# Optimization experiments

Measured on AMD Instinct MI355X. Metric: run time of the kernel, lower is better.

The kernel has to match this reference:

```python
import jax, jax.numpy as jnp
import numpy as np

S = 41          # seq_len
D_IN = 1280
D_OUT = 1024
HEADS = 4
HC = D_OUT // HEADS
EPS = 1e-5

# ---- static edge construction (faithful to the torch code, incl. duplicate edges) ----

def _local_edges(s, window=1):
    e = []
    for i in range(s):
        for j in range(max(0, i - window), min(s, i + window + 1)):
            if i != j:
                e += [(i, j), (j, i)]
    return np.array(e, dtype=np.int32).T

def _region_edges(s):
    e = []
    step = s // 3
    for st in range(0, s, step):
        blk = range(st, min(st + step, s))
        for i in blk:
            for j in blk:
                if i != j:
                    e += [(i, j), (j, i)]
    return np.array(e, dtype=np.int32).T

def _global_edges(s):
    r, c = np.triu_indices(s, 1)  # torch.combinations: (i, j) with i < j
    return np.stack([r, c]).astype(np.int32)

def _batch_edges(e, b, s):
    off = np.arange(b, dtype=np.int32) * s
    return (e[:, None, :] + off[None, :, None]).reshape(2, -1)

_LOCAL = _local_edges(S)
_REGION = _region_edges(S)
_GLOBAL = _global_edges(S)

# ---- layer primitives ----

def _layernorm(x, g, b):
    mu = x.mean(-1, keepdims=True)
    v = ((x - mu) ** 2).mean(-1, keepdims=True)
    return (x - mu) / jnp.sqrt(v + EPS) * g + b

def _gcn(x, w, b, src, tgt, n):
    # PyG GCNConv: x' = D^-1/2 (A + I) D^-1/2 (x W) + b
    h = x @ w
    sl = jnp.arange(n, dtype=src.dtype)
    s = jnp.concatenate([src, sl]); t = jnp.concatenate([tgt, sl])
    deg = jax.ops.segment_sum(jnp.ones(t.shape, h.dtype), t, n)
    dinv = jnp.where(deg > 0, jax.lax.rsqrt(jnp.maximum(deg, 1.0)), 0.0)
    norm = dinv[s] * dinv[t]
    return jax.ops.segment_sum(h[s] * norm[:, None], t, n) + b

def _gat(x, w, a_src, a_dst, b, src, tgt, n):
    # PyG GATConv (shared lin, self loops, leaky_relu 0.2, softmax over incoming edges)
    h = (x @ w).reshape(n, HEADS, HC)
    sl = jnp.arange(n, dtype=src.dtype)
    s = jnp.concatenate([src, sl]); t = jnp.concatenate([tgt, sl])
    al_s = (h * a_src).sum(-1)  # [n, H]
    al_d = (h * a_dst).sum(-1)
    e = jax.nn.leaky_relu(al_s[s] + al_d[t], 0.2)  # [E, H]
    m = jax.ops.segment_max(e, t, n)
    ex = jnp.exp(e - m[t])
    den = jax.ops.segment_sum(ex, t, n)
    alpha = ex / den[t]
    out = jax.ops.segment_sum(h[s] * alpha[:, :, None], t, n)
    return out.reshape(n, HEADS * HC) + b

def _sage(x, wl, bl, wr, src, tgt, n):
    # PyG SAGEConv: mean-aggregate neighbors, plus root transform
    cnt = jax.ops.segment_sum(jnp.ones(src.shape, x.dtype), tgt, n)
    agg = jax.ops.segment_sum(x[src], tgt, n) / jnp.maximum(cnt, 1.0)[:, None]
    return agg @ wl + bl + x @ wr


def setup_inputs() -> dict:
    key = jax.random.key(0)
    ks = jax.random.split(key, 16)
    sc = 0.02
    f32 = jnp.float32
    inp = {
        'x': jax.random.normal(ks[0], (512, S, D_IN), f32),
        'att_w': jax.random.normal(ks[1], (D_IN, 1), f32) * sc,
        'att_b': jnp.zeros((1,), f32),
        'gcn_w': jax.random.normal(ks[2], (D_IN, D_OUT), f32) * sc,
        'gcn_b': jnp.zeros((D_OUT,), f32),
        'sn_g': jnp.ones((D_OUT,), f32), 'sn_b': jnp.zeros((D_OUT,), f32),
        'gat_w': jax.random.normal(ks[3], (D_IN, D_OUT), f32) * sc,
        'gat_as': jax.random.normal(ks[4], (HEADS, HC), f32) * sc,
        'gat_ad': jax.random.normal(ks[5], (HEADS, HC), f32) * sc,
        'gat_b': jnp.zeros((D_OUT,), f32),
        'mn_g': jnp.ones((D_OUT,), f32), 'mn_b': jnp.zeros((D_OUT,), f32),
        'sage_wl': jax.random.normal(ks[6], (D_IN, D_OUT), f32) * sc,
        'sage_bl': jnp.zeros((D_OUT,), f32),
        'sage_wr': jax.random.normal(ks[7], (D_IN, D_OUT), f32) * sc,
        'fp_w1': jax.random.normal(ks[8], (D_IN, 512), f32) * sc,
        'fp_b1': jnp.zeros((512,), f32),
        'fp_w2': jax.random.normal(ks[9], (512, S), f32) * sc,
        'fp_b2': jnp.zeros((S,), f32),
        'dn_g': jnp.ones((D_OUT,), f32), 'dn_b': jnp.zeros((D_OUT,), f32),
        'gate_w': jax.random.normal(ks[10], (3 * D_OUT, 3), f32) * sc,
        'gate_b': jnp.zeros((3,), f32),
    }
    return inp


def reference(x, att_w, att_b, gcn_w, gcn_b, sn_g, sn_b, gat_w, gat_as, gat_ad, gat_b,
              mn_g, mn_b, sage_wl, sage_bl, sage_wr, fp_w1, fp_b1, fp_w2, fp_b2,
              dn_g, dn_b, gate_w, gate_b):
    B = x.shape[0]
    N = B * S
    le = jnp.asarray(_batch_edges(_LOCAL, B, S))
    re = jnp.asarray(_batch_edges(_REGION, B, S))
    ge = jnp.asarray(_batch_edges(_GLOBAL, B, S))

    xf = x.reshape(N, D_IN)
    # shallow: local gating -> GCN -> LN
    enhanced = xf * jax.nn.sigmoid(xf @ att_w + att_b)
    shallow = _gcn(enhanced, gcn_w, gcn_b, le[0], le[1], N)
    shallow = _layernorm(shallow.reshape(B, S, D_OUT), sn_g, sn_b)
    # medium: GAT over region blocks -> LN
    gat = _gat(xf, gat_w, gat_as[None], gat_ad[None], gat_b, re[0], re[1], N)
    gat = _layernorm(gat.reshape(B, S, D_OUT), mn_g, mn_b)
    # deep: learned propagation mixing, SAGE over global edges -> LN
    pw = jax.nn.softmax(jax.nn.relu(x @ fp_w1 + fp_b1) @ fp_w2 + fp_b2, axis=-1)  # [B,S,S]
    sage_in = jnp.einsum('bij,bjd->bid', pw, x).reshape(N, D_IN)
    sage = _sage(sage_in, sage_wl, sage_bl, sage_wr, ge[0], ge[1], N)
    sage = _layernorm(sage.reshape(B, S, D_OUT), dn_g, dn_b)
    # gated branch mixing
    combined = jnp.concatenate([shallow, gat, sage], axis=-1)
    gates = jax.nn.softmax(combined @ gate_w + gate_b, axis=-1)
    total = gates[..., 0:1] * shallow + gates[..., 1:2] * gat + gates[..., 2:3] * sage
    return (shallow, gat, total)
```

## Files before the change

kernel.cpp:

```cpp
#include <hip/hip_runtime.h>
#include <math.h>

static constexpr int S    = 41;
static constexpr int DIN  = 1280;
static constexpr int DOUT = 1024;
static constexpr int HEADS = 4;
static constexpr int HC   = 256;

typedef __attribute__((ext_vector_type(4))) float f32x4;
typedef __attribute__((ext_vector_type(8))) short short8;

__device__ __forceinline__ ushort f2bf(float f) {
  uint u = __float_as_uint(f);
  uint r = u + 0x7fffu + ((u >> 16) & 1u);
  return (ushort)(r >> 16);
}
__device__ __forceinline__ float bf2f(ushort u) {
  return __uint_as_float(((uint)u) << 16);
}

__device__ __forceinline__ void gload16(const ushort* g, ushort* l) {
  __builtin_amdgcn_global_load_lds((const __attribute__((address_space(1))) void*)g,
                                   (__attribute__((address_space(3))) void*)l, 16, 0, 0);
}

#define FENCE() asm volatile("" ::: "memory")


__device__ __forceinline__ float warpReduceSum(float v) {
#pragma unroll
  for (int off = 32; off; off >>= 1) v += __shfl_down(v, off);
  return v;
}

__device__ __forceinline__ void blockReduce6(float* v) {
  __shared__ float red6[6][4];
  int w = threadIdx.x >> 6, lane = threadIdx.x & 63;
#pragma unroll
  for (int r = 0; r < 6; ++r) v[r] = warpReduceSum(v[r]);
  __syncthreads();
  if (lane == 0) {
#pragma unroll
    for (int r = 0; r < 6; ++r) red6[r][w] = v[r];
  }
  __syncthreads();
#pragma unroll
  for (int r = 0; r < 6; ++r)
    v[r] = red6[r][0] + red6[r][1] + red6[r][2] + red6[r][3];
}

__device__ __forceinline__ void blockReduce3v(float* v) {
  __shared__ float red3[3][4];
  int w = threadIdx.x >> 6, lane = threadIdx.x & 63;
#pragma unroll
  for (int r = 0; r < 3; ++r) v[r] = warpReduceSum(v[r]);
  __syncthreads();
  if (lane == 0) {
#pragma unroll
    for (int r = 0; r < 3; ++r) red3[r][w] = v[r];
  }
  __syncthreads();
#pragma unroll
  for (int r = 0; r < 3; ++r)
    v[r] = red3[r][0] + red3[r][1] + red3[r][2] + red3[r][3];
}


__global__ __launch_bounds__(256) void cvtsig_kernel(
    const float4* __restrict__ x, const float* __restrict__ att_w,
    const float* __restrict__ att_b, ushort4* __restrict__ xb, float* __restrict__ sig)
{
  int row  = blockIdx.x * 4 + (threadIdx.x >> 6);
  int lane = threadIdx.x & 63;
  const float4* xr = x + (size_t)row * (DIN / 4);
  const float4* wr = (const float4*)att_w;
  ushort4* xo = xb + (size_t)row * (DIN / 4);
  float acc = 0.f;
#pragma unroll
  for (int k = 0; k < DIN / 4 / 64; ++k) {
    float4 a = xr[lane + k * 64];
    float4 w = wr[lane + k * 64];
    acc += a.x * w.x + a.y * w.y + a.z * w.z + a.w * w.w;
    ushort4 o;
    o.x = f2bf(a.x); o.y = f2bf(a.y); o.z = f2bf(a.z); o.w = f2bf(a.w);
    xo[lane + k * 64] = o;
  }
  acc = warpReduceSum(acc);
  if (lane == 0) sig[row] = 1.f / (1.f + expf(-(acc + att_b[0])));
}


__global__ __launch_bounds__(256) void wcvt_kernel(const float* __restrict__ W,
                                                   ushort* __restrict__ out,
                                                   int K, int N, int ostride, int koff) {
  __shared__ float t[32][33];
  int n0 = blockIdx.x * 32, k0 = blockIdx.y * 32;
  int tx = threadIdx.x & 31, ty = threadIdx.x >> 5;
#pragma unroll
  for (int r = 0; r < 4; ++r) {
    int k = ty + r * 8;
    t[k][tx] = W[(size_t)(k0 + k) * N + n0 + tx];
  }
  __syncthreads();
#pragma unroll
  for (int r = 0; r < 4; ++r) {
    int nn = ty + r * 8;
    out[(size_t)(n0 + nn) * ostride + koff + k0 + tx] = f2bf(t[tx][nn]);
  }
}

__global__ __launch_bounds__(256) void w2cvt_kernel(const float* __restrict__ w2,
                                                    ushort* __restrict__ wpw) {
  int idx = blockIdx.x * 256 + threadIdx.x;
  int n = idx >> 9, k = idx & 511;
  wpw[idx] = (n < S) ? f2bf(w2[(size_t)k * S + n]) : (ushort)0;
}


struct Epi {
  void* dst[5];
  const float* bias[5];
  int nend[5];
  int ld[5];
  int relu[5];
  const float* rs;
};


__global__ __launch_bounds__(512, 1) void gemm8p(
    const ushort* __restrict__ A, const ushort* __restrict__ Bt, int K, int nb, Epi e)
{
  __shared__ __align__(16) ushort As[4 * 8192];
  __shared__ __align__(16) ushort Bs[4 * 8192];

  int wg;
  {
    const int nwg = gridDim.x;
    const int bid = blockIdx.x;
    const int xcd = bid & 7, lin = bid >> 3;
    const int q = nwg >> 3, r = nwg & 7;
    wg = (xcd < r) ? (xcd * (q + 1) + lin) : (r * (q + 1) + (xcd - r) * q + lin);
  }
  const int bm = (wg / nb) * 256;
  const int bn = (wg % nb) * 256;

  const int tid  = threadIdx.x;
  const int wv   = tid >> 6;
  const int lane = tid & 63;
  const int l16  = lane & 15;
  const int l4   = lane >> 4;
  const int m0   = (wv >> 2) * 128;
  const int n0   = (wv & 3) * 64;

  const int rd0 = wv * 16 + (lane >> 2);
  const int rd1 = 128 + wv * 16 + (lane >> 2);
  const int cs0 = ((lane & 3) - ((rd0 >> 1) & 3)) & 3;
  const int cs1 = ((lane & 3) - ((rd1 >> 1) & 3)) & 3;

  auto stageA = [&](int h, int Tt) {
    int kof = Tt * 64 + (h & 1) * 32;
    gload16(A + (size_t)(bm + rd0) * K + kof + cs0 * 8, &As[h * 8192 + wv * 512]);
    gload16(A + (size_t)(bm + rd1) * K + kof + cs1 * 8, &As[h * 8192 + (8 + wv) * 512]);
  };
  auto stageB = [&](int h, int Tt) {
    int kof = Tt * 64 + (h & 1) * 32;
    gload16(Bt + (size_t)(bn + rd0) * K + kof + cs0 * 8, &Bs[h * 8192 + wv * 512]);
    gload16(Bt + (size_t)(bn + rd1) * K + kof + cs1 * 8, &Bs[h * 8192 + (8 + wv) * 512]);
  };

  const int rchunk = ((l4 + ((l16 >> 1) & 3)) & 3) * 8;

  f32x4 acc[8][4];
#pragma unroll
  for (int i = 0; i < 8; ++i)
#pragma unroll
    for (int j = 0; j < 4; ++j) acc[i][j] = (f32x4)0.f;

  const int NT = K >> 6;

  stageA(0, 0); stageB(0, 0);
  stageA(1, 0); stageB(1, 0);
  stageA(2, 1); stageB(2, 1);
  asm volatile("s_waitcnt vmcnt(8)" ::: "memory");
  __builtin_amdgcn_s_barrier();
  FENCE();

  for (int T = 0; T < NT; ++T) {
    const int db = T & 1;
    const int hA = db * 2;
    const int hB = db * 2 + 1;
    short8 a[4], b[4];

#pragma unroll
    for (int i = 0; i < 4; ++i)
      a[i] = *reinterpret_cast<const short8*>(&As[hA * 8192 + (m0 + i * 16 + l16) * 32 + rchunk]);
#pragma unroll
    for (int j = 0; j < 4; ++j)
      b[j] = *reinterpret_cast<const short8*>(&Bs[hA * 8192 + (n0 + j * 16 + l16) * 32 + rchunk]);
    if (T + 1 < NT) stageA((db ^ 1) * 2 + 1, T + 1);
    FENCE(); __builtin_amdgcn_s_barrier(); FENCE();
    __builtin_amdgcn_s_setprio(1);
#pragma unroll
    for (int i = 0; i < 4; ++i)
#pragma unroll
      for (int j = 0; j < 4; ++j)
        acc[i][j] = __builtin_amdgcn_mfma_f32_16x16x32_bf16(a[i], b[j], acc[i][j], 0, 0, 0);
    __builtin_amdgcn_s_setprio(0);
    FENCE(); __builtin_amdgcn_s_barrier(); FENCE();

#pragma unroll
    for (int i = 0; i < 4; ++i)
      a[i] = *reinterpret_cast<const short8*>(&As[hA * 8192 + (m0 + 64 + i * 16 + l16) * 32 + rchunk]);
    if (T + 1 < NT) {
      stageB((db ^ 1) * 2 + 1, T + 1);
      asm volatile("s_waitcnt vmcnt(8)" ::: "memory");
    } else {
      asm volatile("s_waitcnt vmcnt(0)" ::: "memory");
    }
    FENCE(); __builtin_amdgcn_s_barrier(); FENCE();
    __builtin_amdgcn_s_setprio(1);
#pragma unroll
    for (int i = 0; i < 4; ++i)
#pragma unroll
      for (int j = 0; j < 4; ++j)
        acc[4 + i][j] = __builtin_amdgcn_mfma_f32_16x16x32_bf16(a[i], b[j], acc[4 + i][j], 0, 0, 0);
    __builtin_amdgcn_s_setprio(0);
    FENCE(); __builtin_amdgcn_s_barrier(); FENCE();

#pragma unroll
    for (int i = 0; i < 4; ++i)
      a[i] = *reinterpret_cast<const short8*>(&As[hB * 8192 + (m0 + i * 16 + l16) * 32 + rchunk]);
#pragma unroll
    for (int j = 0; j < 4; ++j)
      b[j] = *reinterpret_cast<const short8*>(&Bs[hB * 8192 + (n0 + j * 16 + l16) * 32 + rchunk]);
    if (T + 2 < NT) stageA(hA, T + 2);
    FENCE(); __builtin_amdgcn_s_barrier(); FENCE();
    __builtin_amdgcn_s_setprio(1);
#pragma unroll
    for (int i = 0; i < 4; ++i)
#pragma unroll
      for (int j = 0; j < 4; ++j)
        acc[i][j] = __builtin_amdgcn_mfma_f32_16x16x32_bf16(a[i], b[j], acc[i][j], 0, 0, 0);
    __builtin_amdgcn_s_setprio(0);
    FENCE(); __builtin_amdgcn_s_barrier(); FENCE();

#pragma unroll
    for (int i = 0; i < 4; ++i)
      a[i] = *reinterpret_cast<const short8*>(&As[hB * 8192 + (m0 + 64 + i * 16 + l16) * 32 + rchunk]);
    if (T + 2 < NT) {
      stageB(hA, T + 2);
      asm volatile("s_waitcnt vmcnt(8)" ::: "memory");
    } else if (T + 1 < NT) {
      asm volatile("s_waitcnt vmcnt(4)" ::: "memory");
    }
    FENCE(); __builtin_amdgcn_s_barrier(); FENCE();
    __builtin_amdgcn_s_setprio(1);
#pragma unroll
    for (int i = 0; i < 4; ++i)
#pragma unroll
      for (int j = 0; j < 4; ++j)
        acc[4 + i][j] = __builtin_amdgcn_mfma_f32_16x16x32_bf16(a[i], b[j], acc[4 + i][j], 0, 0, 0);
    __builtin_amdgcn_s_setprio(0);
    FENCE(); __builtin_amdgcn_s_barrier(); FENCE();
  }

  void* dstv; const float* bias; const float* rs = nullptr; int ldc, cb, relu;
  if (bn < e.nend[0])      { dstv = e.dst[0]; ldc = e.ld[0]; cb = bn;             bias = e.bias[0]; relu = e.relu[0]; rs = e.rs; }
  else if (bn < e.nend[1]) { dstv = e.dst[1]; ldc = e.ld[1]; cb = bn - e.nend[0]; bias = e.bias[1]; relu = e.relu[1]; }
  else if (bn < e.nend[2]) { dstv = e.dst[2]; ldc = e.ld[2]; cb = bn - e.nend[1]; bias = e.bias[2]; relu = e.relu[2]; }
  else if (bn < e.nend[3]) { dstv = e.dst[3]; ldc = e.ld[3]; cb = bn - e.nend[2]; bias = e.bias[3]; relu = e.relu[3]; }
  else                     { dstv = e.dst[4]; ldc = e.ld[4]; cb = bn - e.nend[3]; bias = e.bias[4]; relu = e.relu[4]; }

#pragma unroll
  for (int i = 0; i < 8; ++i) {
    int mbase = bm + m0 + i * 16 + l4 * 4;
    float rsv[4];
#pragma unroll
    for (int r = 0; r < 4; ++r) rsv[r] = rs ? rs[mbase + r] : 1.f;
#pragma unroll
    for (int j = 0; j < 4; ++j) {
      int col = cb + n0 + j * 16 + l16;
      float bv = bias ? bias[col] : 0.f;
#pragma unroll
      for (int r = 0; r < 4; ++r) {
        float t = acc[i][j][r] * rsv[r] + bv;
        if (relu) t = fmaxf(t, 0.f);
        ((ushort*)dstv)[(size_t)(mbase + r) * ldc + col] = f2bf(t);
      }
    }
  }
}


template<bool F32OUT>
__global__ __launch_bounds__(256) void gemm_bf16(
    const ushort* __restrict__ A, const ushort* __restrict__ Bt, int K, int nb, Epi e)
{
  __shared__ __align__(16) ushort As[3][128 * 32];
  __shared__ __align__(16) ushort Bs[3][128 * 32];

  const int bid = blockIdx.x;
  const int bm  = (bid / nb) * 128;
  const int bn  = (bid % nb) * 128;

  const int tid  = threadIdx.x;
  const int w    = tid >> 6;
  const int lane = tid & 63;
  const int l16  = lane & 15;
  const int l4   = lane >> 4;
  const int m0   = (w >> 1) * 64;
  const int n0   = (w & 1) * 64;

  const int rloc = lane >> 2;
  const int cpos = lane & 3;
  const int cdat = (cpos - (rloc >> 1)) & 3;
  const int srow = w * 32 + rloc;
  const int scol = cdat * 8;

  f32x4 acc[4][4];
#pragma unroll
  for (int i = 0; i < 4; ++i)
#pragma unroll
    for (int j = 0; j < 4; ++j) acc[i][j] = (f32x4)0.f;

  const ushort* pA0 = A  + (size_t)(bm + srow) * K + scol;
  const ushort* pA1 = A  + (size_t)(bm + srow + 16) * K + scol;
  const ushort* pB0 = Bt + (size_t)(bn + srow) * K + scol;
  const ushort* pB1 = Bt + (size_t)(bn + srow + 16) * K + scol;

  auto stage = [&](int buf, int kt) {
    gload16(pA0 + kt, &As[buf][w * 1024]);
    gload16(pA1 + kt, &As[buf][w * 1024 + 512]);
    gload16(pB0 + kt, &Bs[buf][w * 1024]);
    gload16(pB1 + kt, &Bs[buf][w * 1024 + 512]);
  };

  const int rchunk = ((l4 + (l16 >> 1)) & 3) * 8;

  const int nsteps = K >> 5;
  stage(0, 0); stage(1, 32); stage(2, 64);

  for (int t = 0; t < nsteps; ++t) {
    if (t == 0)                asm volatile("s_waitcnt vmcnt(8)" ::: "memory");
    else if (t == nsteps - 1)  asm volatile("s_waitcnt vmcnt(0)" ::: "memory");
    else                       asm volatile("s_waitcnt vmcnt(4)" ::: "memory");
    __builtin_amdgcn_s_barrier();
    FENCE();

    if (t >= 1 && t + 2 < nsteps) stage((t + 2) % 3, (t + 2) * 32);

    const int cur = t % 3;
    short8 a[4], b[4];
#pragma unroll
    for (int i = 0; i < 4; ++i)
      a[i] = *reinterpret_cast<const short8*>(&As[cur][(m0 + i * 16 + l16) * 32 + rchunk]);
#pragma unroll
    for (int j = 0; j < 4; ++j)
      b[j] = *reinterpret_cast<const short8*>(&Bs[cur][(n0 + j * 16 + l16) * 32 + rchunk]);
    __builtin_amdgcn_s_setprio(1);
#pragma unroll
    for (int i = 0; i < 4; ++i)
#pragma unroll
      for (int j = 0; j < 4; ++j)
        acc[i][j] = __builtin_amdgcn_mfma_f32_16x16x32_bf16(a[i], b[j], acc[i][j], 0, 0, 0);
    __builtin_amdgcn_s_setprio(0);
  }

  void* dstv; const float* bias; const float* rs = nullptr; int ldc, cb, relu;
  if (bn < e.nend[0])      { dstv = e.dst[0]; ldc = e.ld[0]; cb = bn;             bias = e.bias[0]; relu = e.relu[0]; rs = e.rs; }
  else if (bn < e.nend[1]) { dstv = e.dst[1]; ldc = e.ld[1]; cb = bn - e.nend[0]; bias = e.bias[1]; relu = e.relu[1]; }
  else if (bn < e.nend[2]) { dstv = e.dst[2]; ldc = e.ld[2]; cb = bn - e.nend[1]; bias = e.bias[2]; relu = e.relu[2]; }
  else if (bn < e.nend[3]) { dstv = e.dst[3]; ldc = e.ld[3]; cb = bn - e.nend[2]; bias = e.bias[3]; relu = e.relu[3]; }
  else                     { dstv = e.dst[4]; ldc = e.ld[4]; cb = bn - e.nend[3]; bias = e.bias[4]; relu = e.relu[4]; }

#pragma unroll
  for (int i = 0; i < 4; ++i) {
    int mbase = bm + m0 + i * 16 + l4 * 4;
    float rsv[4];
#pragma unroll
    for (int r = 0; r < 4; ++r) rsv[r] = rs ? rs[mbase + r] : 1.f;
#pragma unroll
    for (int j = 0; j < 4; ++j) {
      int col = cb + n0 + j * 16 + l16;
      float bv = bias ? bias[col] : 0.f;
#pragma unroll
      for (int r = 0; r < 4; ++r) {
        float t = acc[i][j][r] * rsv[r] + bv;
        if (relu) t = fmaxf(t, 0.f);
        if (F32OUT) ((float*)dstv)[(size_t)(mbase + r) * ldc + col] = t;
        else        ((ushort*)dstv)[(size_t)(mbase + r) * ldc + col] = f2bf(t);
      }
    }
  }
}


__global__ __launch_bounds__(256) void pwprep_kernel(
    const float* __restrict__ fp2, const float* __restrict__ fp_b2,
    float* __restrict__ pc)
{
  int b = blockIdx.x;
  int tid = threadIdx.x, wv = tid >> 6, lane = tid & 63;
  __shared__ float pws[S][S];
  for (int i = wv; i < S; i += 4) {
    float v = (lane < S) ? (fp2[(size_t)(b * S + i) * 128 + lane] + fp_b2[lane]) : -1e30f;
    float m = v;
#pragma unroll
    for (int off = 32; off; off >>= 1) m = fmaxf(m, __shfl_xor(m, off));
    float e = (lane < S) ? expf(v - m) : 0.f;
    float sum = e;
#pragma unroll
    for (int off = 32; off; off >>= 1) sum += __shfl_xor(sum, off);
    if (lane < S) {
      float p = e / sum;
      pws[i][lane] = p;
      pc[((size_t)b * S + i) * 128 + lane] = p;
    }
  }
  __syncthreads();
  if (tid < S) {
    float run = 0.f;
    for (int i = 0; i < S; ++i) {
      pc[((size_t)b * S + i) * 128 + 64 + tid] = (i > 0) ? run / (float)i : 0.f;
      run += pws[i][tid];
    }
  }
}


__global__ __launch_bounds__(256) void mixc_kernel(
    const float* __restrict__ pc, const ushort* __restrict__ xr,
    const ushort* __restrict__ xl, const float* __restrict__ sage_bl,
    ushort* __restrict__ hbuf)
{
  int b  = blockIdx.y;
  int d0 = blockIdx.x * 256;
  int tid = threadIdx.x;

  float xrv[S], xlv[S];
  const ushort* xrp = xr + (size_t)(b * S) * DOUT + d0 + tid;
  const ushort* xlp = xl + (size_t)(b * S) * DOUT + d0 + tid;
#pragma unroll
  for (int j = 0; j < S; ++j) {
    xrv[j] = bf2f(xrp[(size_t)j * DOUT]);
    xlv[j] = bf2f(xlp[(size_t)j * DOUT]);
  }
  float bl = sage_bl[d0 + tid];
  ushort* op = hbuf + (size_t)(b * S) * DOUT + d0 + tid;
  const float* pcb = pc + (size_t)(b * S) * 128;
  for (int i = 0; i < S; ++i) {
    const float* row = pcb + (size_t)i * 128;
    float acc = bl;
#pragma unroll
    for (int j = 0; j < S; ++j)
      acc += row[j] * xrv[j] + row[64 + j] * xlv[j];
    op[(size_t)i * DOUT] = f2bf(acc);
  }
}


__device__ __forceinline__ float dinv_local(int j) {
  return rsqrtf((j == 0 || j == S - 1) ? 3.f : 5.f);
}

__global__ __launch_bounds__(256) void tail_fused(
    const ushort* __restrict__ gcnh, const ushort* __restrict__ Cgat,
    const ushort* __restrict__ hbuf,
    const float* __restrict__ gcn_b, const float* __restrict__ sn_g, const float* __restrict__ sn_b,
    const float* __restrict__ gat_as, const float* __restrict__ gat_ad, const float* __restrict__ gat_b,
    const float* __restrict__ mn_g, const float* __restrict__ mn_b,
    const float* __restrict__ dn_g, const float* __restrict__ dn_b,
    const float* __restrict__ gw, const float* __restrict__ gb,
    float* __restrict__ out, int N)
{
  int b  = blockIdx.x >> 2;
  int rb = blockIdx.x & 3;
  int lo = rb * 13;
  int cnt = (rb < 3) ? 13 : 2;
  size_t OUT = (size_t)N * DOUT;
  int tid = threadIdx.x;
  int wv = tid >> 6, lane = tid & 63;
  int d0 = tid * 4;
  int head = tid >> 6;

  __shared__ __align__(16) ushort hs[13][DOUT];
  __shared__ float alpha[13][13][HEADS];
  __shared__ float als_l[13][HEADS], ald_l[13][HEADS];

  for (int r = 0; r < cnt; ++r) {
    const ushort4* src = (const ushort4*)(Cgat + (size_t)(b * S + lo + r) * DOUT);
    ((ushort4*)hs[r])[tid] = src[tid];
  }
  __syncthreads();

  {
    const float4* a4 = (const float4*)(gat_as + wv * HC);
    const float4* d4 = (const float4*)(gat_ad + wv * HC);
    float4 av = a4[lane], dv = d4[lane];
    for (int s = 0; s < cnt; ++s) {
      ushort4 hv4 = ((const ushort4*)&hs[s][wv * HC])[lane];
      float h0 = bf2f(hv4.x), h1 = bf2f(hv4.y), h2 = bf2f(hv4.z), h3 = bf2f(hv4.w);
      float a = h0 * av.x + h1 * av.y + h2 * av.z + h3 * av.w;
      float d = h0 * dv.x + h1 * dv.y + h2 * dv.z + h3 * dv.w;
      a = warpReduceSum(a);
      d = warpReduceSum(d);
      if (lane == 0) { als_l[s][wv] = a; ald_l[s][wv] = d; }
    }
  }
  __syncthreads();

  if (tid < cnt * HEADS) {
    int t = tid >> 2, hd = tid & 3;
    float myald = ald_l[t][hd];
    float m = -1e30f;
    for (int s = 0; s < cnt; ++s) {
      float v = als_l[s][hd] + myald;
      v = (v > 0.f) ? v : 0.2f * v;
      m = fmaxf(m, v);
    }
    float den = 0.f;
    for (int s = 0; s < cnt; ++s) {
      float v = als_l[s][hd] + myald;
      v = (v > 0.f) ? v : 0.2f * v;
      float ev = expf(v - m) * ((s == t) ? 1.f : 2.f);
      alpha[t][s][hd] = ev;
      den += ev;
    }
    float inv = 1.f / den;
    for (int s = 0; s < cnt; ++s) alpha[t][s][hd] *= inv;
  }
  __syncthreads();

  float4 gcnb4 = *(const float4*)(gcn_b + d0);
  float4 sng4  = *(const float4*)(sn_g + d0);
  float4 snb4  = *(const float4*)(sn_b + d0);
  float4 gatb4 = *(const float4*)(gat_b + d0);
  float4 mng4  = *(const float4*)(mn_g + d0);
  float4 mnb4  = *(const float4*)(mn_b + d0);
  float4 dng4  = *(const float4*)(dn_g + d0);
  float4 dnb4  = *(const float4*)(dn_b + d0);
  float gwsh[4][3], gwga[4][3], gwsa[4][3];
#pragma unroll
  for (int q = 0; q < 4; ++q)
#pragma unroll
    for (int c = 0; c < 3; ++c) {
      gwsh[q][c] = gw[(size_t)(d0 + q) * 3 + c];
      gwga[q][c] = gw[(size_t)(DOUT + d0 + q) * 3 + c];
      gwsa[q][c] = gw[(size_t)(2 * DOUT + d0 + q) * 3 + c];
    }

  for (int t = 0; t < cnt; ++t) {
    int i = lo + t;
    size_t n = (size_t)(b * S + i);

    float di = dinv_local(i);
    float wc = di * di;
    float wl = (i > 0)     ? 2.f * di * dinv_local(i - 1) : 0.f;
    float wr = (i < S - 1) ? 2.f * di * dinv_local(i + 1) : 0.f;
    const ushort* hc = gcnh + n * DOUT + d0;
    ushort4 c4  = *(const ushort4*)hc;
    ushort4 lft = (i > 0)     ? *(const ushort4*)(hc - DOUT) : ushort4{0, 0, 0, 0};
    ushort4 rgt = (i < S - 1) ? *(const ushort4*)(hc + DOUT) : ushort4{0, 0, 0, 0};
    const ushort* cp = (const ushort*)&c4;
    const ushort* lp = (const ushort*)&lft;
    const ushort* rp = (const ushort*)&rgt;
    const float* gbp = (const float*)&gcnb4;
    float sh[4];
#pragma unroll
    for (int q = 0; q < 4; ++q)
      sh[q] = wc * bf2f(cp[q]) + wl * bf2f(lp[q]) + wr * bf2f(rp[q]) + gbp[q];

    float ga[4] = {0.f, 0.f, 0.f, 0.f};
    for (int si = 0; si < cnt; ++si) {
      float aj = alpha[t][si][head];
      ushort4 hv = *(const ushort4*)&hs[si][d0];
      ga[0] += aj * bf2f(hv.x);
      ga[1] += aj * bf2f(hv.y);
      ga[2] += aj * bf2f(hv.z);
      ga[3] += aj * bf2f(hv.w);
    }
    const float* gab = (const float*)&gatb4;
#pragma unroll
    for (int q = 0; q < 4; ++q) ga[q] += gab[q];

    ushort4 s4v = *(const ushort4*)(hbuf + n * DOUT + d0);
    const ushort* sp = (const ushort*)&s4v;
    float sa[4];
#pragma unroll
    for (int q = 0; q < 4; ++q) sa[q] = bf2f(sp[q]);

    float red[6] = {0.f, 0.f, 0.f, 0.f, 0.f, 0.f};
#pragma unroll
    for (int q = 0; q < 4; ++q) {
      red[0] += sh[q]; red[1] += sh[q] * sh[q];
      red[2] += ga[q]; red[3] += ga[q] * ga[q];
      red[4] += sa[q]; red[5] += sa[q] * sa[q];
    }
    blockReduce6(red);
    float mu0 = red[0] * (1.f / DOUT), r0 = rsqrtf(red[1] * (1.f / DOUT) - mu0 * mu0 + 1e-5f);
    float mu1 = red[2] * (1.f / DOUT), r1 = rsqrtf(red[3] * (1.f / DOUT) - mu1 * mu1 + 1e-5f);
    float mu2 = red[4] * (1.f / DOUT), r2 = rsqrtf(red[5] * (1.f / DOUT) - mu2 * mu2 + 1e-5f);

    const float* sngp = (const float*)&sng4; const float* snbp = (const float*)&snb4;
    const float* mngp = (const float*)&mng4; const float* mnbp = (const float*)&mnb4;
    const float* dngp = (const float*)&dng4; const float* dnbp = (const float*)&dnb4;
    float shn[4], gan[4], san[4];
#pragma unroll
    for (int q = 0; q < 4; ++q) {
      shn[q] = (sh[q] - mu0) * r0 * sngp[q] + snbp[q];
      gan[q] = (ga[q] - mu1) * r1 * mngp[q] + mnbp[q];
      san[q] = (sa[q] - mu2) * r2 * dngp[q] + dnbp[q];
    }

    float p[3] = {0.f, 0.f, 0.f};
#pragma unroll
    for (int q = 0; q < 4; ++q) {
#pragma unroll
      for (int c = 0; c < 3; ++c)
        p[c] += shn[q] * gwsh[q][c] + gan[q] * gwga[q][c] + san[q] * gwsa[q][c];
    }
    blockReduce3v(p);
    float l0 = p[0] + gb[0], l1 = p[1] + gb[1], l2 = p[2] + gb[2];
    float m = fmaxf(l0, fmaxf(l1, l2));
    float e0 = expf(l0 - m), e1 = expf(l1 - m), e2 = expf(l2 - m);
    float inv = 1.f / (e0 + e1 + e2);
    float g0 = e0 * inv, g1 = e1 * inv, g2 = e2 * inv;

    float4 o0, o1, o2;
    float* o0p = (float*)&o0; float* o1p = (float*)&o1; float* o2p = (float*)&o2;
#pragma unroll
    for (int q = 0; q < 4; ++q) {
      o0p[q] = shn[q];
      o1p[q] = gan[q];
      o2p[q] = g0 * shn[q] + g1 * gan[q] + g2 * san[q];
    }
    *(float4*)(out + n * DOUT + d0)           = o0;
    *(float4*)(out + OUT + n * DOUT + d0)     = o1;
    *(float4*)(out + 2 * OUT + n * DOUT + d0) = o2;
  }
}


extern "C" void kernel_launch(void* const* d_in, const int* in_sizes, int n_in,
                              void* d_out, int out_size, void* d_ws, size_t ws_size,
                              hipStream_t stream) {
  const float* x       = (const float*)d_in[0];
  const float* att_w   = (const float*)d_in[1];
  const float* att_b   = (const float*)d_in[2];
  const float* gcn_w   = (const float*)d_in[3];
  const float* gcn_b   = (const float*)d_in[4];
  const float* sn_g    = (const float*)d_in[5];
  const float* sn_b    = (const float*)d_in[6];
  const float* gat_w   = (const float*)d_in[7];
  const float* gat_as  = (const float*)d_in[8];
  const float* gat_ad  = (const float*)d_in[9];
  const float* gat_b   = (const float*)d_in[10];
  const float* mn_g    = (const float*)d_in[11];
  const float* mn_b    = (const float*)d_in[12];
  const float* sage_wl = (const float*)d_in[13];
  const float* sage_bl = (const float*)d_in[14];
  const float* sage_wr = (const float*)d_in[15];
  const float* fp_w1   = (const float*)d_in[16];
  const float* fp_b1   = (const float*)d_in[17];
  const float* fp_w2   = (const float*)d_in[18];
  const float* fp_b2   = (const float*)d_in[19];
  const float* dn_g    = (const float*)d_in[20];
  const float* dn_b    = (const float*)d_in[21];
  const float* gate_w  = (const float*)d_in[22];
  const float* gate_b  = (const float*)d_in[23];

  const int B = in_sizes[0] / (S * DIN);
  const int N = B * S;
  const int MB  = N / 128;
  const int MB2 = N / 256;
  const int NMEGA = 4608;
  float* out = (float*)d_out;

  char* ws = (char*)d_ws;
  size_t off = 0;
  auto alloc = [&](size_t bytes) { size_t p = off; off += (bytes + 255) & ~(size_t)255; return p; };
  ushort* xb   = (ushort*)(ws + alloc((size_t)N * DIN * 2));
  ushort* Bt   = (ushort*)(ws + alloc((size_t)NMEGA * DIN * 2));
  ushort* wpw  = (ushort*)(ws + alloc((size_t)128 * 512 * 2));
  ushort* gcnh = (ushort*)(ws + alloc((size_t)N * DOUT * 2));
  ushort* Cgat = (ushort*)(ws + alloc((size_t)N * DOUT * 2));
  ushort* xr   = (ushort*)(ws + alloc((size_t)N * DOUT * 2));
  ushort* xl   = (ushort*)(ws + alloc((size_t)N * DOUT * 2));
  ushort* hbuf = (ushort*)(ws + alloc((size_t)N * DOUT * 2));
  float*  fp2  = (float*)(ws + alloc((size_t)N * 128 * 4));
  float*  pc   = (float*)(ws + alloc((size_t)N * 128 * 4));
  float*  sig  = (float*)(ws + alloc((size_t)N * 4));
  ushort* fp1  = hbuf;

  dim3 blk(256);

  cvtsig_kernel<<<N / 4, blk, 0, stream>>>((const float4*)x, att_w, att_b, (ushort4*)xb, sig);
  wcvt_kernel<<<dim3(DOUT / 32, DIN / 32), blk, 0, stream>>>(gcn_w, Bt, DIN, DOUT, DIN, 0);
  wcvt_kernel<<<dim3(DOUT / 32, DIN / 32), blk, 0, stream>>>(gat_w, Bt + (size_t)1024 * DIN, DIN, DOUT, DIN, 0);
  wcvt_kernel<<<dim3(512 / 32, DIN / 32), blk, 0, stream>>>(fp_w1, Bt + (size_t)2048 * DIN, DIN, 512, DIN, 0);
  wcvt_kernel<<<dim3(DOUT / 32, DIN / 32), blk, 0, stream>>>(sage_wr, Bt + (size_t)2560 * DIN, DIN, DOUT, DIN, 0);
  wcvt_kernel<<<dim3(DOUT / 32, DIN / 32), blk, 0, stream>>>(sage_wl, Bt + (size_t)3584 * DIN, DIN, DOUT, DIN, 0);
  w2cvt_kernel<<<dim3(128 * 512 / 256), blk, 0, stream>>>(fp_w2, wpw);

  Epi e1;
  e1.dst[0] = gcnh; e1.dst[1] = Cgat; e1.dst[2] = fp1; e1.dst[3] = xr; e1.dst[4] = xl;
  e1.bias[0] = nullptr; e1.bias[1] = nullptr; e1.bias[2] = fp_b1; e1.bias[3] = nullptr; e1.bias[4] = nullptr;
  e1.nend[0] = 1024; e1.nend[1] = 2048; e1.nend[2] = 2560; e1.nend[3] = 3584; e1.nend[4] = 4608;
  e1.ld[0] = DOUT; e1.ld[1] = DOUT; e1.ld[2] = 512; e1.ld[3] = DOUT; e1.ld[4] = DOUT;
  e1.relu[0] = 0; e1.relu[1] = 0; e1.relu[2] = 1; e1.relu[3] = 0; e1.relu[4] = 0;
  e1.rs = sig;
  gemm8p<<<dim3(MB2 * (NMEGA / 256)), dim3(512), 0, stream>>>(xb, Bt, DIN, NMEGA / 256, e1);

  Epi epw;
  epw.dst[0] = fp2; epw.dst[1] = nullptr; epw.dst[2] = nullptr; epw.dst[3] = nullptr; epw.dst[4] = nullptr;
  epw.bias[0] = nullptr; epw.bias[1] = nullptr; epw.bias[2] = nullptr; epw.bias[3] = nullptr; epw.bias[4] = nullptr;
  epw.nend[0] = 1 << 30; epw.nend[1] = 1 << 30; epw.nend[2] = 1 << 30; epw.nend[3] = 1 << 30; epw.nend[4] = 1 << 30;
  epw.ld[0] = 128; epw.ld[1] = 128; epw.ld[2] = 128; epw.ld[3] = 128; epw.ld[4] = 128;
  epw.relu[0] = 0; epw.relu[1] = 0; epw.relu[2] = 0; epw.relu[3] = 0; epw.relu[4] = 0;
  epw.rs = nullptr;
  gemm_bf16<true><<<dim3(MB), blk, 0, stream>>>(fp1, wpw, 512, 1, epw);

  pwprep_kernel<<<B, blk, 0, stream>>>(fp2, fp_b2, pc);
  mixc_kernel<<<dim3(DOUT / 256, B), blk, 0, stream>>>(pc, xr, xl, sage_bl, hbuf);

  tail_fused<<<B * 4, blk, 0, stream>>>(gcnh, Cgat, hbuf,
                                        gcn_b, sn_g, sn_b,
                                        gat_as, gat_ad, gat_b,
                                        mn_g, mn_b, dn_g, dn_b,
                                        gate_w, gate_b, out, N);
}
```

Baseline: 652.1 us.

## Batch weight conversions, unroll GEMM k-loop by two, and trim reduction barriers

Four weight-transpose launches are merged into one wcvt4 launch that picks its matrix from blockIdx.z. The GEMM main loop is unrolled by two with a constant double-buffer index, and global addresses are precomputed once outside the loop. The final epilogue block reductions use parity-indexed (double-buffered) shared scratch, which drops one __syncthreads per reduction. These target launch overhead, address arithmetic and barrier cost, but the two-way unroll assumes the tile count K/64 is even.

```diff
diff --git a/kernel.cpp b/kernel.cpp
--- a/kernel.cpp
+++ b/kernel.cpp
@@ -31,38 +31,6 @@
 #pragma unroll
   for (int off = 32; off; off >>= 1) v += __shfl_down(v, off);
   return v;
-}
-
-__device__ __forceinline__ void blockReduce6(float* v) {
-  __shared__ float red6[6][4];
-  int w = threadIdx.x >> 6, lane = threadIdx.x & 63;
-#pragma unroll
-  for (int r = 0; r < 6; ++r) v[r] = warpReduceSum(v[r]);
-  __syncthreads();
-  if (lane == 0) {
-#pragma unroll
-    for (int r = 0; r < 6; ++r) red6[r][w] = v[r];
-  }
-  __syncthreads();
-#pragma unroll
-  for (int r = 0; r < 6; ++r)
-    v[r] = red6[r][0] + red6[r][1] + red6[r][2] + red6[r][3];
-}
-
-__device__ __forceinline__ void blockReduce3v(float* v) {
-  __shared__ float red3[3][4];
-  int w = threadIdx.x >> 6, lane = threadIdx.x & 63;
-#pragma unroll
-  for (int r = 0; r < 3; ++r) v[r] = warpReduceSum(v[r]);
-  __syncthreads();
-  if (lane == 0) {
-#pragma unroll
-    for (int r = 0; r < 3; ++r) red3[r][w] = v[r];
-  }
-  __syncthreads();
-#pragma unroll
-  for (int r = 0; r < 3; ++r)
-    v[r] = red3[r][0] + red3[r][1] + red3[r][2] + red3[r][3];
 }
 
 
@@ -90,6 +58,27 @@
 }
 
 
+struct W4 { const float* src[4]; ushort* dst[4]; };
+
+__global__ __launch_bounds__(256) void wcvt4_kernel(W4 w) {
+  __shared__ float t[32][33];
+  const float* W = w.src[blockIdx.z];
+  ushort* out = w.dst[blockIdx.z];
+  int n0 = blockIdx.x * 32, k0 = blockIdx.y * 32;
+  int tx = threadIdx.x & 31, ty = threadIdx.x >> 5;
+#pragma unroll
+  for (int r = 0; r < 4; ++r) {
+    int k = ty + r * 8;
+    t[k][tx] = W[(size_t)(k0 + k) * DOUT + n0 + tx];
+  }
+  __syncthreads();
+#pragma unroll
+  for (int r = 0; r < 4; ++r) {
+    int nn = ty + r * 8;
+    out[(size_t)(n0 + nn) * DIN + k0 + tx] = f2bf(t[tx][nn]);
+  }
+}
+
 __global__ __launch_bounds__(256) void wcvt_kernel(const float* __restrict__ W,
                                                    ushort* __restrict__ out,
                                                    int K, int N, int ostride, int koff) {
@@ -157,15 +146,18 @@
   const int cs0 = ((lane & 3) - ((rd0 >> 1) & 3)) & 3;
   const int cs1 = ((lane & 3) - ((rd1 >> 1) & 3)) & 3;
 
-  auto stageA = [&](int h, int Tt) {
-    int kof = Tt * 64 + (h & 1) * 32;
-    gload16(A + (size_t)(bm + rd0) * K + kof + cs0 * 8, &As[h * 8192 + wv * 512]);
-    gload16(A + (size_t)(bm + rd1) * K + kof + cs1 * 8, &As[h * 8192 + (8 + wv) * 512]);
+  const ushort* gA0 = A  + (size_t)(bm + rd0) * K + cs0 * 8;
+  const ushort* gA1 = A  + (size_t)(bm + rd1) * K + cs1 * 8;
+  const ushort* gB0 = Bt + (size_t)(bn + rd0) * K + cs0 * 8;
+  const ushort* gB1 = Bt + (size_t)(bn + rd1) * K + cs1 * 8;
+
+  auto stageA = [&](int h, int kof) {
+    gload16(gA0 + kof, &As[h * 8192 + wv * 512]);
+    gload16(gA1 + kof, &As[h * 8192 + (8 + wv) * 512]);
   };
-  auto stageB = [&](int h, int Tt) {
-    int kof = Tt * 64 + (h & 1) * 32;
-    gload16(Bt + (size_t)(bn + rd0) * K + kof + cs0 * 8, &Bs[h * 8192 + wv * 512]);
-    gload16(Bt + (size_t)(bn + rd1) * K + kof + cs1 * 8, &Bs[h * 8192 + (8 + wv) * 512]);
+  auto stageB = [&](int h, int kof) {
+    gload16(gB0 + kof, &Bs[h * 8192 + wv * 512]);
+    gload16(gB1 + kof, &Bs[h * 8192 + (8 + wv) * 512]);
   };
 
   const int rchunk = ((l4 + ((l16 >> 1) & 3)) & 3) * 8;
@@ -178,15 +170,14 @@
 
   const int NT = K >> 6;
 
-  stageA(0, 0); stageB(0, 0);
-  stageA(1, 0); stageB(1, 0);
-  stageA(2, 1); stageB(2, 1);
+  stageA(0, 0);  stageB(0, 0);
+  stageA(1, 32); stageB(1, 32);
+  stageA(2, 64); stageB(2, 64);
   asm volatile("s_waitcnt vmcnt(8)" ::: "memory");
   __builtin_amdgcn_s_barrier();
   FENCE();
 
-  for (int T = 0; T < NT; ++T) {
-    const int db = T & 1;
+  auto tileBody = [&](int T, const int db) {
     const int hA = db * 2;
     const int hB = db * 2 + 1;
     short8 a[4], b[4];
@@ -197,7 +188,7 @@
 #pragma unroll
     for (int j = 0; j < 4; ++j)
       b[j] = *reinterpret_cast<const short8*>(&Bs[hA * 8192 + (n0 + j * 16 + l16) * 32 + rchunk]);
-    if (T + 1 < NT) stageA((db ^ 1) * 2 + 1, T + 1);
+    if (T + 1 < NT) stageA((db ^ 1) * 2 + 1, (T + 1) * 64 + 32);
     FENCE(); __builtin_amdgcn_s_barrier(); FENCE();
     __builtin_amdgcn_s_setprio(1);
 #pragma unroll
@@ -212,7 +203,7 @@
     for (int i = 0; i < 4; ++i)
       a[i] = *reinterpret_cast<const short8*>(&As[hA * 8192 + (m0 + 64 + i * 16 + l16) * 32 + rchunk]);
     if (T + 1 < NT) {
-      stageB((db ^ 1) * 2 + 1, T + 1);
+      stageB((db ^ 1) * 2 + 1, (T + 1) * 64 + 32);
       asm volatile("s_waitcnt vmcnt(8)" ::: "memory");
     } else {
       asm volatile("s_waitcnt vmcnt(0)" ::: "memory");
@@ -233,7 +224,7 @@
 #pragma unroll
     for (int j = 0; j < 4; ++j)
       b[j] = *reinterpret_cast<const short8*>(&Bs[hB * 8192 + (n0 + j * 16 + l16) * 32 + rchunk]);
-    if (T + 2 < NT) stageA(hA, T + 2);
+    if (T + 2 < NT) stageA(hA, (T + 2) * 64);
     FENCE(); __builtin_amdgcn_s_barrier(); FENCE();
     __builtin_amdgcn_s_setprio(1);
 #pragma unroll
@@ -248,7 +239,7 @@
     for (int i = 0; i < 4; ++i)
       a[i] = *reinterpret_cast<const short8*>(&As[hB * 8192 + (m0 + 64 + i * 16 + l16) * 32 + rchunk]);
     if (T + 2 < NT) {
-      stageB(hA, T + 2);
+      stageB(hA, (T + 2) * 64);
       asm volatile("s_waitcnt vmcnt(8)" ::: "memory");
     } else if (T + 1 < NT) {
       asm volatile("s_waitcnt vmcnt(4)" ::: "memory");
@@ -262,6 +253,11 @@
         acc[4 + i][j] = __builtin_amdgcn_mfma_f32_16x16x32_bf16(a[i], b[j], acc[4 + i][j], 0, 0, 0);
     __builtin_amdgcn_s_setprio(0);
     FENCE(); __builtin_amdgcn_s_barrier(); FENCE();
+  };
+
+  for (int T = 0; T < NT; T += 2) {
+    tileBody(T, 0);
+    tileBody(T + 1, 1);
   }
 
   void* dstv; const float* bias; const float* rs = nullptr; int ldc, cb, relu;
@@ -486,6 +482,8 @@
   __shared__ __align__(16) ushort hs[13][DOUT];
   __shared__ float alpha[13][13][HEADS];
   __shared__ float als_l[13][HEADS], ald_l[13][HEADS];
+  __shared__ float red6[2][6][4];
+  __shared__ float red3[2][3][4];
 
   for (int r = 0; r < cnt; ++r) {
     const ushort4* src = (const ushort4*)(Cgat + (size_t)(b * S + lo + r) * DOUT);
@@ -552,6 +550,7 @@
   for (int t = 0; t < cnt; ++t) {
     int i = lo + t;
     size_t n = (size_t)(b * S + i);
+    int par = t & 1;
 
     float di = dinv_local(i);
     float wc = di * di;
@@ -596,7 +595,17 @@
       red[2] += ga[q]; red[3] += ga[q] * ga[q];
       red[4] += sa[q]; red[5] += sa[q] * sa[q];
     }
-    blockReduce6(red);
+#pragma unroll
+    for (int r = 0; r < 6; ++r) red[r] = warpReduceSum(red[r]);
+    if (lane == 0) {
+#pragma unroll
+      for (int r = 0; r < 6; ++r) red6[par][r][wv] = red[r];
+    }
+    __syncthreads();
+#pragma unroll
+    for (int r = 0; r < 6; ++r)
+      red[r] = red6[par][r][0] + red6[par][r][1] + red6[par][r][2] + red6[par][r][3];
+
     float mu0 = red[0] * (1.f / DOUT), r0 = rsqrtf(red[1] * (1.f / DOUT) - mu0 * mu0 + 1e-5f);
     float mu1 = red[2] * (1.f / DOUT), r1 = rsqrtf(red[3] * (1.f / DOUT) - mu1 * mu1 + 1e-5f);
     float mu2 = red[4] * (1.f / DOUT), r2 = rsqrtf(red[5] * (1.f / DOUT) - mu2 * mu2 + 1e-5f);
@@ -619,7 +628,17 @@
       for (int c = 0; c < 3; ++c)
         p[c] += shn[q] * gwsh[q][c] + gan[q] * gwga[q][c] + san[q] * gwsa[q][c];
     }
-    blockReduce3v(p);
+#pragma unroll
+    for (int r = 0; r < 3; ++r) p[r] = warpReduceSum(p[r]);
+    if (lane == 0) {
+#pragma unroll
+      for (int r = 0; r < 3; ++r) red3[par][r][wv] = p[r];
+    }
+    __syncthreads();
+#pragma unroll
+    for (int r = 0; r < 3; ++r)
+      p[r] = red3[par][r][0] + red3[par][r][1] + red3[par][r][2] + red3[par][r][3];
+
     float l0 = p[0] + gb[0], l1 = p[1] + gb[1], l2 = p[2] + gb[2];
     float m = fmaxf(l0, fmaxf(l1, l2));
     float e0 = expf(l0 - m), e1 = expf(l1 - m), e2 = expf(l2 - m);
@@ -695,11 +714,13 @@
   dim3 blk(256);
 
   cvtsig_kernel<<<N / 4, blk, 0, stream>>>((const float4*)x, att_w, att_b, (ushort4*)xb, sig);
-  wcvt_kernel<<<dim3(DOUT / 32, DIN / 32), blk, 0, stream>>>(gcn_w, Bt, DIN, DOUT, DIN, 0);
-  wcvt_kernel<<<dim3(DOUT / 32, DIN / 32), blk, 0, stream>>>(gat_w, Bt + (size_t)1024 * DIN, DIN, DOUT, DIN, 0);
+  W4 w4;
+  w4.src[0] = gcn_w;  w4.dst[0] = Bt;
+  w4.src[1] = gat_w;  w4.dst[1] = Bt + (size_t)1024 * DIN;
+  w4.src[2] = sage_wr; w4.dst[2] = Bt + (size_t)2560 * DIN;
+  w4.src[3] = sage_wl; w4.dst[3] = Bt + (size_t)3584 * DIN;
+  wcvt4_kernel<<<dim3(DOUT / 32, DIN / 32, 4), blk, 0, stream>>>(w4);
   wcvt_kernel<<<dim3(512 / 32, DIN / 32), blk, 0, stream>>>(fp_w1, Bt + (size_t)2048 * DIN, DIN, 512, DIN, 0);
-  wcvt_kernel<<<dim3(DOUT / 32, DIN / 32), blk, 0, stream>>>(sage_wr, Bt + (size_t)2560 * DIN, DIN, DOUT, DIN, 0);
-  wcvt_kernel<<<dim3(DOUT / 32, DIN / 32), blk, 0, stream>>>(sage_wl, Bt + (size_t)3584 * DIN, DIN, DOUT, DIN, 0);
   w2cvt_kernel<<<dim3(128 * 512 / 256), blk, 0, stream>>>(fp_w2, wpw);
 
   Epi e1;
```

Result: no change. 640.2 us, median of 3 (-1.8%).
